# Optimization experiments

Hardware: AMD Instinct MI355X
Metric: run time of the kernel (lower is better)

## Reference

```python
import jax, jax.numpy as jnp
import numpy as np
import math

# batch, in-channels, attention_maps, heads, features (== input height), frames
B, C, M, H, F_, W = 2, 8, 8, 8, 256, 512
HD = F_ // H  # head dim = 32


def conv2d(x, w, pad):
    return jax.lax.conv_general_dilated(x, w, (1, 1), pad,
                                        dimension_numbers=('NCHW', 'OIHW', 'NCHW'))


def rotary(x):
    # lucidrains-style interleaved rotary over last dim; x: [..., seq, d]
    d, seq = x.shape[-1], x.shape[-2]
    inv_freq = 1.0 / (10000.0 ** (jnp.arange(0, d, 2, dtype=jnp.float32) / d))
    freqs = jnp.arange(seq, dtype=jnp.float32)[:, None] * inv_freq[None, :]  # [seq, d/2]
    freqs = jnp.repeat(freqs, 2, axis=-1)  # [seq, d], each freq repeated for the (x1,x2) pair
    cos, sin = jnp.cos(freqs), jnp.sin(freqs)
    x1, x2 = x[..., 0::2], x[..., 1::2]
    xr = jnp.stack((-x2, x1), axis=-1).reshape(x.shape)  # rotate_half
    return x * cos + xr * sin


def setup_inputs() -> dict:
    key = jax.random.key(0)
    ks = jax.random.split(key, 12)
    s = 0.02
    return {
        'x': jax.random.normal(ks[0], (B, C, F_, W), jnp.float32),
        'prev_qk': jax.random.normal(ks[1], (B, M, H, W, W), jnp.float32) * 0.1,
        'q_c1': jax.random.normal(ks[2], (M, C, 3, 3), jnp.float32) * s,
        'q_lin': jax.random.normal(ks[3], (M, F_, F_), jnp.float32) * s,
        'q_c2': jax.random.normal(ks[4], (M, M, 1, 3), jnp.float32) * s,
        'k_c1': jax.random.normal(ks[5], (M, C, 3, 3), jnp.float32) * s,
        'k_lin': jax.random.normal(ks[6], (M, F_, F_), jnp.float32) * s,
        'k_c2': jax.random.normal(ks[7], (M, M, 1, 3), jnp.float32) * s,
        'v_c1': jax.random.normal(ks[8], (M, C, 3, 3), jnp.float32) * s,
        'v_lin': jax.random.normal(ks[9], (M, F_, F_), jnp.float32) * s,
        'v_c2': jax.random.normal(ks[10], (M, M, 1, 3), jnp.float32) * s,
        'o_w': jax.random.normal(ks[11], (M, F_, F_), jnp.float32) * s,
    }


def _proj(x, wc1, wl, wc2):
    h = conv2d(x, wc1, [(1, 1), (1, 1)])        # [B,M,F,W] 3x3 conv, no bias
    h = jnp.einsum('bcfw,cgf->bcgw', h, wl)      # MultichannelLinear: per-map linear on feature dim
    h = conv2d(h, wc2, [(0, 0), (1, 1)])         # (1,3) conv along frames
    return h


def _heads(t):
    # [B,M,F,W] -> transpose(2,3) -> [B,M,W,F] -> [B,M,W,H,HD] -> [B,M,H,W,HD]
    return t.transpose(0, 1, 3, 2).reshape(B, M, W, H, HD).transpose(0, 1, 3, 2, 4)


def reference(x, prev_qk, q_c1, q_lin, q_c2, k_c1, k_lin, k_c2, v_c1, v_lin, v_c2, o_w):
    q = rotary(_heads(_proj(x, q_c1, q_lin, q_c2)))
    k = rotary(_heads(_proj(x, k_c1, k_lin, k_c2)))
    v = _heads(_proj(x, v_c1, v_lin, v_c2))
    # scaled by sqrt(h) where h == input height == features (non-standard)
    qk = jnp.einsum('bmhqd,bmhkd->bmhqk', q, k) / math.sqrt(F_) + prev_qk
    a = jnp.einsum('bmhqk,bmhkd->bmhqd', jax.nn.softmax(qk, axis=-1), v)
    a = a.transpose(0, 1, 3, 2, 4).reshape(B, M, W, F_).transpose(0, 1, 3, 2)  # [B,M,F,W]
    out = jnp.einsum('bcfw,cgf->bcgw', a, o_w)  # o_proj MultichannelLinear
    return (out, qk)
```

## Files before the change

### kernel.cpp

```cpp
#include <hip/hip_runtime.h>

#define B 2
#define C 8
#define M 8
#define H 8
#define F 256
#define W 512
#define HD 32
#define MFF (M * F * F)

typedef __attribute__((ext_vector_type(8))) __bf16 bf16x8;
typedef __attribute__((ext_vector_type(4))) float f32x4;

__device__ __forceinline__ unsigned short f2bf(float f) {
    unsigned int u = __float_as_uint(f);
    return (unsigned short)((u + 0x7fffu + ((u >> 16) & 1u)) >> 16);
}

__device__ __forceinline__ unsigned int packsplit(float v) {
    unsigned short h = f2bf(v);
    float hf = __uint_as_float((unsigned int)h << 16);
    unsigned short lo = f2bf(v - hf);
    return (unsigned int)h | ((unsigned int)lo << 16);
}

__global__ __launch_bounds__(256) void wsplit_kernel(const float* __restrict__ w0,
                                                     const float* __restrict__ w1,
                                                     const float* __restrict__ w2,
                                                     const float* __restrict__ w3,
                                                     unsigned short* __restrict__ hi) {
    int idx = blockIdx.x * 256 + threadIdx.x;
    int set = idx >> 17;
    int off = (idx & 131071) * 4;
    const float* src = (set == 0) ? w0 : (set == 1) ? w1 : (set == 2) ? w2 : w3;
    float4 v = *(const float4*)&src[off];
    unsigned short* hp = hi + (size_t)set * MFF + off;
    unsigned short* lp = hp + 4 * MFF;
    ushort4 hv, lv;
    float x;
    x = v.x; hv.x = f2bf(x); lv.x = f2bf(x - __uint_as_float((unsigned)hv.x << 16));
    x = v.y; hv.y = f2bf(x); lv.y = f2bf(x - __uint_as_float((unsigned)hv.y << 16));
    x = v.z; hv.z = f2bf(x); lv.z = f2bf(x - __uint_as_float((unsigned)hv.z << 16));
    x = v.w; hv.w = f2bf(x); lv.w = f2bf(x - __uint_as_float((unsigned)hv.w << 16));
    *(ushort4*)hp = hv;
    *(ushort4*)lp = lv;
}

__global__ __launch_bounds__(256) void conv1_kernel(const float* __restrict__ x,
                                                    const float* __restrict__ w0,
                                                    const float* __restrict__ w1,
                                                    const float* __restrict__ w2,
                                                    unsigned int* __restrict__ out) {
    int t = threadIdx.x;
    int zb = blockIdx.z;
    int b = zb >> 3, m = zb & 7;
    int wi = blockIdx.x * 64 + (t & 63);
    int f0t = blockIdx.y * 32 + (t >> 6) * 8;
    const float* xb = x + (size_t)b * C * F * W;
    const float* wq = w0 + m * 72;
    const float* wk = w1 + m * 72;
    const float* wv = w2 + m * 72;
    int wm = (wi > 0) ? wi - 1 : 0;
    int wp = (wi < W - 1) ? wi + 1 : W - 1;
    bool e0 = (wi > 0), e1 = (wi < W - 1);
    float acc[3][8] = {};
    for (int i = 0; i < 8; ++i) {
        const float* xi = xb + (size_t)i * F * W;
        float v0[10], v1[10], v2[10];
        #pragma unroll
        for (int rr = 0; rr < 10; ++rr) {
            int ff = f0t + rr - 1;
            if (ff >= 0 && ff < F) {
                const float* xr = xi + (size_t)ff * W;
                float a = xr[wm], bb = xr[wi], c = xr[wp];
                v0[rr] = e0 ? a : 0.f;
                v1[rr] = bb;
                v2[rr] = e1 ? c : 0.f;
            } else {
                v0[rr] = 0.f; v1[rr] = 0.f; v2[rr] = 0.f;
            }
        }
        #pragma unroll
        for (int p = 0; p < 3; ++p) {
            const float* wt = ((p == 0) ? wq : (p == 1) ? wk : wv) + i * 9;
            #pragma unroll
            for (int df = 0; df < 3; ++df) {
                float s0 = wt[df * 3 + 0];
                float s1 = wt[df * 3 + 1];
                float s2 = wt[df * 3 + 2];
                #pragma unroll
                for (int ff = 0; ff < 8; ++ff)
                    acc[p][ff] += v0[ff + df] * s0 + v1[ff + df] * s1 + v2[ff + df] * s2;
            }
        }
    }
    #pragma unroll
    for (int p = 0; p < 3; ++p) {
        size_t zo = (size_t)(p * 16 + zb) * F;
        #pragma unroll
        for (int ff = 0; ff < 8; ++ff)
            out[(zo + f0t + ff) * W + wi] = packsplit(acc[p][ff]);
    }
}

__global__ __launch_bounds__(256) void lin_kernel(const unsigned int* __restrict__ in32,
                                                  const unsigned short* __restrict__ whA,
                                                  const unsigned short* __restrict__ whB,
                                                  const unsigned short* __restrict__ whC,
                                                  float* __restrict__ out) {
    __shared__ unsigned int BsH[64][20];
    __shared__ unsigned int BsL[64][20];
    int t = threadIdx.x;
    int z = blockIdx.z;
    int proj = z >> 4, m = z & 7;
    const unsigned short* wh = ((proj == 0) ? whA : (proj == 1) ? whB : whC) + (size_t)m * F * F;
    const unsigned short* wl = wh + 4 * MFF;
    const unsigned int* ib = in32 + (size_t)z * F * W;
    float* ob = out + (size_t)z * F * W;
    int g0 = blockIdx.y * 64, wb0 = blockIdx.x * 64;
    int wv = t >> 6, l = t & 63, lr = l & 15, lg = l >> 4;
    int wgr = wv >> 1, wgc = wv & 1;
    int sp = t & 15;
    int sg = t >> 4;

    uint4 ra, rb;
    ra = *(const uint4*)&ib[(size_t)(2 * sp) * W + wb0 + sg * 4];
    rb = *(const uint4*)&ib[(size_t)(2 * sp + 1) * W + wb0 + sg * 4];

    f32x4 acc[2][2];
    acc[0][0] = (f32x4)0.f; acc[0][1] = (f32x4)0.f;
    acc[1][0] = (f32x4)0.f; acc[1][1] = (f32x4)0.f;

    for (int s = 0; s < 8; ++s) {
        int f0 = s * 32;
        if (s) __syncthreads();
        unsigned int aw[4] = {ra.x, ra.y, ra.z, ra.w};
        unsigned int bw[4] = {rb.x, rb.y, rb.z, rb.w};
        #pragma unroll
        for (int j = 0; j < 4; ++j) {
            BsH[sg * 4 + j][sp] = (aw[j] & 0xFFFFu) | (bw[j] << 16);
            BsL[sg * 4 + j][sp] = (aw[j] >> 16) | (bw[j] & 0xFFFF0000u);
        }
        __syncthreads();
        if (s < 7) {
            ra = *(const uint4*)&ib[(size_t)(f0 + 32 + 2 * sp) * W + wb0 + sg * 4];
            rb = *(const uint4*)&ib[(size_t)(f0 + 32 + 2 * sp + 1) * W + wb0 + sg * 4];
        }
        bf16x8 ah[2], al[2], bh[2], bl[2];
        #pragma unroll
        for (int ti = 0; ti < 2; ++ti) {
            size_t ar = (size_t)(g0 + wgr * 32 + ti * 16 + lr) * F + f0 + lg * 8;
            ah[ti] = *(const bf16x8*)&wh[ar];
            al[ti] = *(const bf16x8*)&wl[ar];
        }
        #pragma unroll
        for (int tj = 0; tj < 2; ++tj) {
            int wc = wgc * 32 + tj * 16 + lr;
            bh[tj] = *(const bf16x8*)((const unsigned short*)&BsH[wc][0] + lg * 8);
            bl[tj] = *(const bf16x8*)((const unsigned short*)&BsL[wc][0] + lg * 8);
        }
        #pragma unroll
        for (int ti = 0; ti < 2; ++ti)
            #pragma unroll
            for (int tj = 0; tj < 2; ++tj) {
                acc[ti][tj] = __builtin_amdgcn_mfma_f32_16x16x32_bf16(ah[ti], bh[tj], acc[ti][tj], 0, 0, 0);
                acc[ti][tj] = __builtin_amdgcn_mfma_f32_16x16x32_bf16(ah[ti], bl[tj], acc[ti][tj], 0, 0, 0);
                acc[ti][tj] = __builtin_amdgcn_mfma_f32_16x16x32_bf16(al[ti], bh[tj], acc[ti][tj], 0, 0, 0);
            }
    }
    #pragma unroll
    for (int ti = 0; ti < 2; ++ti)
        #pragma unroll
        for (int tj = 0; tj < 2; ++tj)
            #pragma unroll
            for (int r = 0; r < 4; ++r) {
                int g = g0 + wgr * 32 + ti * 16 + lg * 4 + r;
                int w = wb0 + wgc * 32 + tj * 16 + lr;
                ob[(size_t)g * W + w] = acc[ti][tj][r];
            }
}

__global__ __launch_bounds__(256) void conv2_heads_kernel(const float* __restrict__ in,
                                                          const float* __restrict__ w0c,
                                                          const float* __restrict__ w1c,
                                                          const float* __restrict__ w2c,
                                                          unsigned short* __restrict__ outp) {
    __shared__ float wl[192];
    __shared__ float Ot[64][65];
    int t = threadIdx.x;
    int z = blockIdx.z;
    int proj = z >> 4, bz = z & 15;
    int b = bz >> 3, o = bz & 7;
    const float* wt = (proj == 0) ? w0c : (proj == 1) ? w1c : w2c;
    int do_rot = (proj < 2);
    if (t < 192) wl[t] = wt[t];
    __syncthreads();
    int f0 = blockIdx.y * 64, w0 = blockIdx.x * 64;
    const float* ib = in + ((size_t)proj * 16 + (size_t)b * M) * F * W;
    int ww = t & 63, fq = (t >> 6) * 16;
    int w = w0 + ww;
    for (int ff = 0; ff < 16; ++ff) {
        int f = f0 + fq + ff;
        float acc = 0.f;
        #pragma unroll
        for (int i = 0; i < 8; ++i) {
            const float* r = ib + ((size_t)i * F + f) * W + w;
            float v0 = (w - 1 >= 0) ? r[-1] : 0.f;
            float v1 = r[0];
            float v2 = (w + 1 < W) ? r[1] : 0.f;
            const float* wr = &wl[(o * 8 + i) * 3];
            acc += v0 * wr[0] + v1 * wr[1] + v2 * wr[2];
        }
        Ot[fq + ff][ww] = acc;
    }
    __syncthreads();
    size_t zbase = (size_t)z * H * W * HD;
    if (do_rot) {
        for (int k = 0; k < 16; ++k) {
            int idx = k * 256 + t;
            int ddh = idx & 63;
            int wi = idx >> 6;
            int f = f0 + ddh;
            int h = f >> 5, d = f & 31;
            float e  = Ot[ddh & ~1][wi];
            float od = Ot[ddh | 1][wi];
            int jp = d >> 1;
            float invf = exp2f(-(float)jp * 0.83048202372184058f);
            float th = (float)(w0 + wi) * invf;
            float cs = __cosf(th), sn = __sinf(th);
            float val = (d & 1) ? (od * cs + e * sn) : (e * cs - od * sn);
            outp[zbase + ((size_t)h * W + (w0 + wi)) * HD + d] = f2bf(val);
        }
    } else {
        for (int k = 0; k < 16; ++k) {
            int idx = k * 256 + t;
            int wi = idx & 63;
            int ddh = idx >> 6;
            int f = f0 + ddh;
            int h = f >> 5, d = f & 31;
            outp[zbase + ((size_t)(h * HD + d)) * W + (w0 + wi)] = f2bf(Ot[ddh][wi]);
        }
    }
}

__global__ __launch_bounds__(256) void attn_kernel(const unsigned short* __restrict__ qb,
                                                   const unsigned short* __restrict__ kb,
                                                   const unsigned short* __restrict__ vtb,
                                                   const float* __restrict__ prev,
                                                   float* __restrict__ qk,
                                                   unsigned int* __restrict__ abuf) {
    __shared__ __align__(16) unsigned short VsT[32 * 520];
    __shared__ __align__(16) unsigned short PT[4][16 * 72];
    int t = threadIdx.x;
    int l = t & 63, wv = t >> 6;
    int lr = l & 15, lg = l >> 4;
    int w0 = blockIdx.x * 64;
    int bmh = blockIdx.y;
    const unsigned short* Q  = qb  + (size_t)bmh * W * HD;
    const unsigned short* K  = kb  + (size_t)bmh * W * HD;
    const unsigned short* VT = vtb + (size_t)bmh * HD * W;
    const float* P0 = prev + (size_t)bmh * W * W;
    float* QK = qk + (size_t)bmh * W * W;
    int bm = bmh >> 3, h = bmh & 7;
    unsigned int* A = abuf + ((size_t)bm * F + h * HD) * W;

    #pragma unroll
    for (int it = 0; it < 8; ++it) {
        int e16 = it * 256 + t;
        int hd = e16 >> 6, w8 = (e16 & 63) * 8;
        *(uint4*)&VsT[hd * 520 + w8] = *(const uint4*)&VT[(size_t)hd * W + w8];
    }
    int qrow = w0 + wv * 16;
    bf16x8 qf = *(const bf16x8*)&Q[(size_t)(qrow + lr) * HD + lg * 8];

    float m_i[4], l_i[4];
    f32x4 accA[2];
    #pragma unroll
    for (int r = 0; r < 4; ++r) { m_i[r] = -3.0e38f; l_i[r] = 0.f; }
    accA[0] = (f32x4)0.f;
    accA[1] = (f32x4)0.f;

    __syncthreads();

    bf16x8 kfA[4], kfB[4];
    f32x4 pvA[4], pvB[4];

    auto issue = [&](bf16x8 (&kf)[4], f32x4 (&pv)[4], int c) {
        int j0 = c * 64;
        #pragma unroll
        for (int ct = 0; ct < 4; ++ct)
            kf[ct] = *(const bf16x8*)&K[(size_t)(j0 + ct * 16 + lr) * HD + lg * 8];
        #pragma unroll
        for (int ct = 0; ct < 4; ++ct) {
            const float* pr = &P0[(size_t)(qrow + lg * 4) * W + j0 + ct * 16 + lr];
            #pragma unroll
            for (int r = 0; r < 4; ++r) pv[ct][r] = pr[(size_t)r * W];
        }
    };

    auto step = [&](bf16x8 (&kf)[4], f32x4 (&pv)[4], int c) {
        int j0 = c * 64;
        f32x4 sc[4];
        #pragma unroll
        for (int ct = 0; ct < 4; ++ct)
            sc[ct] = __builtin_amdgcn_mfma_f32_16x16x32_bf16(qf, kf[ct], pv[ct] * 16.f, 0, 0, 0);
        float sv[4][4];
        #pragma unroll
        for (int ct = 0; ct < 4; ++ct) {
            #pragma unroll
            for (int r = 0; r < 4; ++r) {
                sv[ct][r] = sc[ct][r] * 0.0625f;
                QK[(size_t)(qrow + lg * 4 + r) * W + j0 + ct * 16 + lr] = sv[ct][r];
            }
        }
        float p[4][4];
        #pragma unroll
        for (int r = 0; r < 4; ++r) {
            float cm = fmaxf(fmaxf(sv[0][r], sv[1][r]), fmaxf(sv[2][r], sv[3][r]));
            #pragma unroll
            for (int off = 1; off < 16; off <<= 1) cm = fmaxf(cm, __shfl_xor(cm, off));
            float mn = fmaxf(m_i[r], cm);
            float alpha = __expf(m_i[r] - mn);
            m_i[r] = mn;
            float rs = 0.f;
            #pragma unroll
            for (int ct = 0; ct < 4; ++ct) { p[ct][r] = __expf(sv[ct][r] - mn); rs += p[ct][r]; }
            #pragma unroll
            for (int off = 1; off < 16; off <<= 1) rs += __shfl_xor(rs, off);
            l_i[r] = l_i[r] * alpha + rs;
            accA[0][r] *= alpha;
            accA[1][r] *= alpha;
        }
        unsigned short* PTw = &PT[wv][0];
        #pragma unroll
        for (int ct = 0; ct < 4; ++ct)
            #pragma unroll
            for (int r = 0; r < 4; ++r)
                PTw[(lg * 4 + r) * 72 + ct * 16 + lr] = f2bf(p[ct][r]);
        asm volatile("s_waitcnt lgkmcnt(0)" ::: "memory");
        __builtin_amdgcn_sched_barrier(0);
        bf16x8 pf[2];
        pf[0] = *(const bf16x8*)&PTw[lr * 72 + lg * 8];
        pf[1] = *(const bf16x8*)&PTw[lr * 72 + 32 + lg * 8];
        #pragma unroll
        for (int ks = 0; ks < 2; ++ks)
            #pragma unroll
            for (int ct2 = 0; ct2 < 2; ++ct2) {
                bf16x8 vf = *(const bf16x8*)&VsT[(ct2 * 16 + lr) * 520 + j0 + ks * 32 + lg * 8];
                accA[ct2] = __builtin_amdgcn_mfma_f32_16x16x32_bf16(pf[ks], vf, accA[ct2], 0, 0, 0);
            }
    };

    issue(kfA, pvA, 0);
    #pragma unroll
    for (int cc = 0; cc < 4; ++cc) {
        issue(kfB, pvB, 2 * cc + 1);
        step(kfA, pvA, 2 * cc);
        if (cc < 3) issue(kfA, pvA, 2 * cc + 2);
        step(kfB, pvB, 2 * cc + 1);
    }

    float inv[4];
    #pragma unroll
    for (int r = 0; r < 4; ++r) inv[r] = 1.f / l_i[r];
    float* Otf = (float*)&PT[wv][0];
    asm volatile("s_waitcnt lgkmcnt(0)" ::: "memory");
    #pragma unroll
    for (int ct2 = 0; ct2 < 2; ++ct2)
        #pragma unroll
        for (int r = 0; r < 4; ++r)
            Otf[(lg * 4 + r) * 33 + ct2 * 16 + lr] = accA[ct2][r] * inv[r];
    asm volatile("s_waitcnt lgkmcnt(0)" ::: "memory");
    __builtin_amdgcn_sched_barrier(0);
    #pragma unroll
    for (int k = 0; k < 8; ++k) {
        int flat = k * 64 + l;
        int woff = flat & 15, d = flat >> 4;
        A[(size_t)d * W + w0 + wv * 16 + woff] = packsplit(Otf[woff * 33 + d]);
    }
}

extern "C" void kernel_launch(void* const* d_in, const int* in_sizes, int n_in,
                              void* d_out, int out_size, void* d_ws, size_t ws_size,
                              hipStream_t stream) {
    const float* x    = (const float*)d_in[0];
    const float* prev = (const float*)d_in[1];
    const float* qc1  = (const float*)d_in[2];
    const float* qlin = (const float*)d_in[3];
    const float* qc2  = (const float*)d_in[4];
    const float* kc1  = (const float*)d_in[5];
    const float* klin = (const float*)d_in[6];
    const float* kc2  = (const float*)d_in[7];
    const float* vc1  = (const float*)d_in[8];
    const float* vlin = (const float*)d_in[9];
    const float* vc2  = (const float*)d_in[10];
    const float* ow   = (const float*)d_in[11];
    float* out0  = (float*)d_out;
    float* qkout = out0 + (size_t)B * M * F * W;
    float* ws = (float*)d_ws;
    size_t n = (size_t)B * M * F * W;
    float* r1 = ws;
    float* r2 = ws + 3 * n;
    unsigned int* r1u = (unsigned int*)r1;
    unsigned int* r2u = (unsigned int*)r2;
    unsigned short* qkv16 = (unsigned short*)r1;
    unsigned short* whi = (unsigned short*)(ws + 6 * n);

    dim3 blk(256);
    dim3 gsplit(2048), gconv1(8, 8, 16), glin3(8, 4, 48), gconv2(8, 4, 48);
    dim3 gattn(8, 128), glin1(8, 4, 16);

    wsplit_kernel<<<gsplit, blk, 0, stream>>>(qlin, klin, vlin, ow, whi);
    conv1_kernel<<<gconv1, blk, 0, stream>>>(x, qc1, kc1, vc1, r1u);
    lin_kernel<<<glin3, blk, 0, stream>>>(r1u, whi, whi + MFF, whi + 2 * MFF, r2);
    conv2_heads_kernel<<<gconv2, blk, 0, stream>>>(r2, qc2, kc2, vc2, qkv16);
    attn_kernel<<<gattn, blk, 0, stream>>>(qkv16, qkv16 + n, qkv16 + 2 * n, prev, qkout, r2u);
    lin_kernel<<<glin1, blk, 0, stream>>>(r2u, whi + 3 * MFF, whi + 3 * MFF, whi + 3 * MFF, out0);
}
```

Measured before the change: 398.8 us.

## Vectorize conv2 taps, read V directly from global, use nontemporal prev/qk access

```diff
diff --git a/kernel.cpp b/kernel.cpp
--- a/kernel.cpp
+++ b/kernel.cpp
@@ -197,21 +197,31 @@
     __syncthreads();
     int f0 = blockIdx.y * 64, w0 = blockIdx.x * 64;
     const float* ib = in + ((size_t)proj * 16 + (size_t)b * M) * F * W;
-    int ww = t & 63, fq = (t >> 6) * 16;
-    int w = w0 + ww;
-    for (int ff = 0; ff < 16; ++ff) {
-        int f = f0 + fq + ff;
-        float acc = 0.f;
+    int wgi = t & 15, fr = t >> 4;
+    int wq = w0 + wgi * 4;
+    bool eL = (wq > 0);
+    bool eR = (wq + 4 < W);
+    #pragma unroll
+    for (int fi = 0; fi < 4; ++fi) {
+        int f = f0 + fr * 4 + fi;
+        float a0 = 0.f, a1 = 0.f, a2 = 0.f, a3 = 0.f;
         #pragma unroll
         for (int i = 0; i < 8; ++i) {
-            const float* r = ib + ((size_t)i * F + f) * W + w;
-            float v0 = (w - 1 >= 0) ? r[-1] : 0.f;
-            float v1 = r[0];
-            float v2 = (w + 1 < W) ? r[1] : 0.f;
+            const float* r = ib + ((size_t)i * F + f) * W + wq;
+            float4 v = *(const float4*)r;
+            float vlft = eL ? r[-1] : 0.f;
+            float vrgt = eR ? r[4] : 0.f;
             const float* wr = &wl[(o * 8 + i) * 3];
-            acc += v0 * wr[0] + v1 * wr[1] + v2 * wr[2];
-        }
-        Ot[fq + ff][ww] = acc;
+            float c0 = wr[0], c1 = wr[1], c2 = wr[2];
+            a0 += vlft * c0 + v.x * c1 + v.y * c2;
+            a1 += v.x  * c0 + v.y * c1 + v.z * c2;
+            a2 += v.y  * c0 + v.z * c1 + v.w * c2;
+            a3 += v.z  * c0 + v.w * c1 + vrgt * c2;
+        }
+        Ot[fr * 4 + fi][wgi * 4 + 0] = a0;
+        Ot[fr * 4 + fi][wgi * 4 + 1] = a1;
+        Ot[fr * 4 + fi][wgi * 4 + 2] = a2;
+        Ot[fr * 4 + fi][wgi * 4 + 3] = a3;
     }
     __syncthreads();
     size_t zbase = (size_t)z * H * W * HD;
@@ -249,7 +259,6 @@
                                                    const float* __restrict__ prev,
                                                    float* __restrict__ qk,
                                                    unsigned int* __restrict__ abuf) {
-    __shared__ __align__(16) unsigned short VsT[32 * 520];
     __shared__ __align__(16) unsigned short PT[4][16 * 72];
     int t = threadIdx.x;
     int l = t & 63, wv = t >> 6;
@@ -264,12 +273,6 @@
     int bm = bmh >> 3, h = bmh & 7;
     unsigned int* A = abuf + ((size_t)bm * F + h * HD) * W;
 
-    #pragma unroll
-    for (int it = 0; it < 8; ++it) {
-        int e16 = it * 256 + t;
-        int hd = e16 >> 6, w8 = (e16 & 63) * 8;
-        *(uint4*)&VsT[hd * 520 + w8] = *(const uint4*)&VT[(size_t)hd * W + w8];
-    }
     int qrow = w0 + wv * 16;
     bf16x8 qf = *(const bf16x8*)&Q[(size_t)(qrow + lr) * HD + lg * 8];
 
@@ -280,8 +283,6 @@
     accA[0] = (f32x4)0.f;
     accA[1] = (f32x4)0.f;
 
-    __syncthreads();
-
     bf16x8 kfA[4], kfB[4];
     f32x4 pvA[4], pvB[4];
 
@@ -294,7 +295,7 @@
         for (int ct = 0; ct < 4; ++ct) {
             const float* pr = &P0[(size_t)(qrow + lg * 4) * W + j0 + ct * 16 + lr];
             #pragma unroll
-            for (int r = 0; r < 4; ++r) pv[ct][r] = pr[(size_t)r * W];
+            for (int r = 0; r < 4; ++r) pv[ct][r] = __builtin_nontemporal_load(&pr[(size_t)r * W]);
         }
     };
 
@@ -304,13 +305,20 @@
         #pragma unroll
         for (int ct = 0; ct < 4; ++ct)
             sc[ct] = __builtin_amdgcn_mfma_f32_16x16x32_bf16(qf, kf[ct], pv[ct] * 16.f, 0, 0, 0);
+        bf16x8 vf[2][2];
+        #pragma unroll
+        for (int ks = 0; ks < 2; ++ks)
+            #pragma unroll
+            for (int ct2 = 0; ct2 < 2; ++ct2)
+                vf[ks][ct2] = *(const bf16x8*)&VT[(size_t)(ct2 * 16 + lr) * W + j0 + ks * 32 + lg * 8];
         float sv[4][4];
         #pragma unroll
         for (int ct = 0; ct < 4; ++ct) {
             #pragma unroll
             for (int r = 0; r < 4; ++r) {
                 sv[ct][r] = sc[ct][r] * 0.0625f;
-                QK[(size_t)(qrow + lg * 4 + r) * W + j0 + ct * 16 + lr] = sv[ct][r];
+                __builtin_nontemporal_store(sv[ct][r],
+                    &QK[(size_t)(qrow + lg * 4 + r) * W + j0 + ct * 16 + lr]);
             }
         }
         float p[4][4];
@@ -345,10 +353,8 @@
         #pragma unroll
         for (int ks = 0; ks < 2; ++ks)
             #pragma unroll
-            for (int ct2 = 0; ct2 < 2; ++ct2) {
-                bf16x8 vf = *(const bf16x8*)&VsT[(ct2 * 16 + lr) * 520 + j0 + ks * 32 + lg * 8];
-                accA[ct2] = __builtin_amdgcn_mfma_f32_16x16x32_bf16(pf[ks], vf, accA[ct2], 0, 0, 0);
-            }
+            for (int ct2 = 0; ct2 < 2; ++ct2)
+                accA[ct2] = __builtin_amdgcn_mfma_f32_16x16x32_bf16(pf[ks], vf[ks][ct2], accA[ct2], 0, 0, 0);
     };
 
     issue(kfA, pvA, 0);
```

Result: slower. 414.2 us (+3.9%).
